# Performance work log

Hardware: AMD Instinct MI355X
Metric: run time of the kernel (lower is better)

The kernel has to match this reference:

```python
import jax, jax.numpy as jnp
import numpy as np
import math

MAX_L = 3
N_NODES, N_RADIAL, N_CHANNEL = 50000, 8, 16


def _build_tables(max_l):
    # Cartesian angular basis (lx,ly,lz) with lx+ly+lz <= max_l, (0,0,0) first.
    l_list = []
    for l in range(max_l + 1):
        for lx in range(l, -1, -1):
            for ly in range(l - lx, -1, -1):
                l_list.append((lx, ly, l - lx - ly))
    idx = {t: i for i, t in enumerate(l_list)}
    # nu=2 combos: per l (slot l-1), sum of multinomial-weighted squares.
    indices, pref, slots = [], [], []
    for l in range(1, max_l + 1):
        for lx in range(l, -1, -1):
            for ly in range(l - lx, -1, -1):
                lz = l - lx - ly
                i = idx[(lx, ly, lz)]
                indices.append([i, i])
                pref.append(math.factorial(l) / (math.factorial(lx) * math.factorial(ly) * math.factorial(lz)))
                slots.append(l - 1)
    return (np.asarray(indices, np.int32), np.asarray(pref, np.float32),
            np.asarray(slots, np.int32), len(l_list))


def setup_inputs() -> dict:
    key = jax.random.key(0)
    indices, pref, slots, n_ang = _build_tables(MAX_L)
    node_attr = jax.random.normal(key, (N_NODES, N_RADIAL, n_ang, N_CHANNEL), dtype=jnp.float32)
    return {
        "node_attr": node_attr,
        "prefactors": jnp.asarray(pref),
        "indices": jnp.asarray(indices),
        "slots": jnp.asarray(slots),
    }


def reference(node_attr, prefactors, indices, slots):
    # node_attr: [N, R, A, C]; indices: [M, 2]; prefactors: [M]; slots: [M]
    n, r, _, c = node_attr.shape
    n_slots = MAX_L  # one slot per order l for nu=2
    g = node_attr[:, :, indices, :]                    # [N, R, M, 2, C] gather
    prod = g[..., 0, :] * g[..., 1, :]                 # product over nu dim
    weighted = prod * prefactors[None, None, :, None]  # prefactor scale
    sym_rest = jnp.zeros((n, r, n_slots, c), node_attr.dtype)
    sym_rest = sym_rest.at[:, :, slots, :].add(weighted)  # scatter_add into slots
    # slot 0 is the raw l=0 channel
    return jnp.concatenate([node_attr[:, :, :1, :], sym_rest], axis=2)
```

## Files before the change

### kernel.cpp

```cpp
#include <hip/hip_runtime.h>


typedef float f32x4 __attribute__((ext_vector_type(4)));

constexpr int N_ANG   = 20;
constexpr int OUT_ANG = 4;

__global__ __launch_bounds__(256) void symmetrizer_kernel(
    const f32x4* __restrict__ in,
    f32x4*       __restrict__ out,
    int nthreads)
{
    int tid = blockIdx.x * blockDim.x + threadIdx.x;
    if (tid >= nthreads) return;

    int row = tid >> 2;
    int c4  = tid & 3;

    const f32x4* ib = in + (size_t)row * (N_ANG * 4) + c4;

    f32x4 v0  = ib[0 * 4],  v1  = ib[1 * 4],  v2  = ib[2 * 4],  v3  = ib[3 * 4];
    f32x4 v4  = ib[4 * 4],  v5  = ib[5 * 4],  v6  = ib[6 * 4],  v7  = ib[7 * 4];
    f32x4 v8  = ib[8 * 4],  v9  = ib[9 * 4],  v10 = ib[10 * 4], v11 = ib[11 * 4];
    f32x4 v12 = ib[12 * 4], v13 = ib[13 * 4], v14 = ib[14 * 4], v15 = ib[15 * 4];
    f32x4 v16 = ib[16 * 4], v17 = ib[17 * 4], v18 = ib[18 * 4], v19 = ib[19 * 4];

    f32x4 s0 = v1 * v1 + v2 * v2 + v3 * v3;

    f32x4 s1 = v4 * v4 + 2.f * (v5 * v5) + 2.f * (v6 * v6)
             + v7 * v7 + 2.f * (v8 * v8) + v9 * v9;

    f32x4 s2 = v10 * v10 + 3.f * (v11 * v11) + 3.f * (v12 * v12)
             + 3.f * (v13 * v13) + 6.f * (v14 * v14) + 3.f * (v15 * v15)
             + v16 * v16 + 3.f * (v17 * v17) + 3.f * (v18 * v18)
             + v19 * v19;

    f32x4* ob = out + (size_t)row * (OUT_ANG * 4) + c4;
    __builtin_nontemporal_store(v0, ob + 0);
    __builtin_nontemporal_store(s0, ob + 4);
    __builtin_nontemporal_store(s1, ob + 8);
    __builtin_nontemporal_store(s2, ob + 12);
}

extern "C" void kernel_launch(void* const* d_in, const int* in_sizes, int n_in,
                              void* d_out, int out_size, void* d_ws, size_t ws_size,
                              hipStream_t stream) {
    const float* node_attr = (const float*)d_in[0];
    float*       out       = (float*)d_out;

    int rows = in_sizes[0] / (N_ANG * 16);
    int nthreads = rows * 4;

    int block = 256;
    int grid  = (nthreads + block - 1) / block;

    symmetrizer_kernel<<<grid, block, 0, stream>>>(
        (const f32x4*)node_attr, (f32x4*)out, nthreads);
}
```

Measured before the change: 115.9 us.

## Stage input rows through LDS with fully coalesced contiguous global loads

```diff
diff --git a/kernel.cpp b/kernel.cpp
--- a/kernel.cpp
+++ b/kernel.cpp
@@ -3,39 +3,63 @@
 
 typedef float f32x4 __attribute__((ext_vector_type(4)));
 
-constexpr int N_ANG   = 20;
-constexpr int OUT_ANG = 4;
+constexpr int ROWS_PB     = 64;
+constexpr int IN_ROW_F4   = 80;
+constexpr int OUT_ROW_F4  = 16;
+constexpr int STAGE_F4    = 76;
+constexpr int LDS_STRIDE_DW = 308;
+constexpr int LOADS_PT    = (ROWS_PB * STAGE_F4) / 256;
 
 __global__ __launch_bounds__(256) void symmetrizer_kernel(
     const f32x4* __restrict__ in,
-    f32x4*       __restrict__ out,
-    int nthreads)
+    f32x4*       __restrict__ out)
 {
-    int tid = blockIdx.x * blockDim.x + threadIdx.x;
-    if (tid >= nthreads) return;
+    extern __shared__ float lds[];
 
-    int row = tid >> 2;
-    int c4  = tid & 3;
+    const int t = threadIdx.x;
+    const size_t base_f4 = (size_t)blockIdx.x * ROWS_PB * IN_ROW_F4;
 
-    const f32x4* ib = in + (size_t)row * (N_ANG * 4) + c4;
+    f32x4 g[LOADS_PT];
+    unsigned rr[LOADS_PT], ww[LOADS_PT];
+#pragma unroll
+    for (int i = 0; i < LOADS_PT; ++i) {
+        unsigned f = (unsigned)(i * 256 + t);
+        unsigned r = f / STAGE_F4;
+        unsigned w = f - r * STAGE_F4;
+        rr[i] = r; ww[i] = w;
+        g[i] = in[base_f4 + r * IN_ROW_F4 + 4 + w];
+    }
+#pragma unroll
+    for (int i = 0; i < LOADS_PT; ++i) {
+        *(f32x4*)&lds[rr[i] * LDS_STRIDE_DW + ww[i] * 4] = g[i];
+    }
 
-    f32x4 v0  = ib[0 * 4],  v1  = ib[1 * 4],  v2  = ib[2 * 4],  v3  = ib[3 * 4];
-    f32x4 v4  = ib[4 * 4],  v5  = ib[5 * 4],  v6  = ib[6 * 4],  v7  = ib[7 * 4];
-    f32x4 v8  = ib[8 * 4],  v9  = ib[9 * 4],  v10 = ib[10 * 4], v11 = ib[11 * 4];
-    f32x4 v12 = ib[12 * 4], v13 = ib[13 * 4], v14 = ib[14 * 4], v15 = ib[15 * 4];
-    f32x4 v16 = ib[16 * 4], v17 = ib[17 * 4], v18 = ib[18 * 4], v19 = ib[19 * 4];
+    const int r  = t >> 2;
+    const int c4 = t & 3;
 
-    f32x4 s0 = v1 * v1 + v2 * v2 + v3 * v3;
+    f32x4 v0 = in[base_f4 + (size_t)r * IN_ROW_F4 + c4];
 
-    f32x4 s1 = v4 * v4 + 2.f * (v5 * v5) + 2.f * (v6 * v6)
-             + v7 * v7 + 2.f * (v8 * v8) + v9 * v9;
+    __syncthreads();
 
-    f32x4 s2 = v10 * v10 + 3.f * (v11 * v11) + 3.f * (v12 * v12)
-             + 3.f * (v13 * v13) + 6.f * (v14 * v14) + 3.f * (v15 * v15)
-             + v16 * v16 + 3.f * (v17 * v17) + 3.f * (v18 * v18)
-             + v19 * v19;
+    const int rb = r * LDS_STRIDE_DW + c4 * 4;
+    f32x4 d[19];
+#pragma unroll
+    for (int k = 0; k < 19; ++k) {
+        d[k] = *(const f32x4*)&lds[rb + k * 16];
+    }
 
-    f32x4* ob = out + (size_t)row * (OUT_ANG * 4) + c4;
+    f32x4 s0 = d[0] * d[0] + d[1] * d[1] + d[2] * d[2];
+
+    f32x4 s1 = d[3] * d[3] + 2.f * (d[4] * d[4]) + 2.f * (d[5] * d[5])
+             + d[6] * d[6] + 2.f * (d[7] * d[7]) + d[8] * d[8];
+
+    f32x4 s2 = d[9] * d[9]  + 3.f * (d[10] * d[10]) + 3.f * (d[11] * d[11])
+             + 3.f * (d[12] * d[12]) + 6.f * (d[13] * d[13])
+             + 3.f * (d[14] * d[14]) + d[15] * d[15]
+             + 3.f * (d[16] * d[16]) + 3.f * (d[17] * d[17])
+             + d[18] * d[18];
+
+    f32x4* ob = out + ((size_t)blockIdx.x * ROWS_PB + r) * OUT_ROW_F4 + c4;
     __builtin_nontemporal_store(v0, ob + 0);
     __builtin_nontemporal_store(s0, ob + 4);
     __builtin_nontemporal_store(s1, ob + 8);
@@ -48,12 +72,10 @@
     const float* node_attr = (const float*)d_in[0];
     float*       out       = (float*)d_out;
 
-    int rows = in_sizes[0] / (N_ANG * 16);
-    int nthreads = rows * 4;
+    int rows   = in_sizes[0] / (20 * 16);
+    int blocks = rows / ROWS_PB;
+    size_t lds_bytes = ROWS_PB * LDS_STRIDE_DW * sizeof(float);
 
-    int block = 256;
-    int grid  = (nthreads + block - 1) / block;
-
-    symmetrizer_kernel<<<grid, block, 0, stream>>>(
-        (const f32x4*)node_attr, (f32x4*)out, nthreads);
+    symmetrizer_kernel<<<blocks, 256, lds_bytes, stream>>>(
+        (const f32x4*)node_attr, (f32x4*)out);
 }
```

New measurement: 110.7 us (median of 2 runs). 4.5% less time.
